# Kernel tuning notes

Measured on AMD Instinct MI355X. Metric: run time of the kernel, lower is better.

The kernel has to match this reference:

```python
import jax, jax.numpy as jnp
import numpy as np

NEG_INF = -1e9

def setup_inputs() -> dict:
    key = jax.random.key(0)
    ks = jax.random.split(key, 6)
    B, M, RNN, H, D = 64, 1024, 1024, 512, 2048
    return {
        "h": jax.random.normal(ks[0], (B, RNN), dtype=jnp.float32),
        "att_feats": jax.random.normal(ks[1], (B, M, D), dtype=jnp.float32),
        "att_mask": jax.random.randint(ks[2], (B, M), 0, 2, dtype=jnp.int32),
        "p_att_feats": jax.random.normal(ks[3], (B, M, H), dtype=jnp.float32),
        "W_ah": jax.random.normal(ks[4], (H, RNN), dtype=jnp.float32) * (1.0 / np.sqrt(RNN)),
        "w_alpha": jax.random.normal(ks[5], (H,), dtype=jnp.float32) * (1.0 / np.sqrt(H)),
    }

def reference(h, att_feats, att_mask, p_att_feats, W_ah, w_alpha):
    # Wah(h): [B, H]
    wah = h @ W_ah.T
    # additive attention energies: tanh(Wah(h)[:, None, :] + p_att_feats) -> [B, M, H]
    e = jnp.tanh(wah[:, None, :] + p_att_feats)
    # project to scalar per region: [B, M]
    logits = jnp.einsum("bmh,h->bm", e, w_alpha)
    logits = jnp.where(att_mask == 0, NEG_INF, logits)
    alpha = jax.nn.softmax(logits, axis=-1)
    # weighted sum of region features: [B, D]
    att = jnp.einsum("bm,bmd->bd", alpha, att_feats)
    return att
```

## Files before the change

kernel.cpp:

```cpp
#include <hip/hip_runtime.h>
#include <math.h>

#define B   64
#define M   1024
#define RNN 1024
#define H   512
#define D   2048
#define NEG_INF -1e9f

#define MBLK   8
#define MCHUNK (M / MBLK)

__device__ __forceinline__ float fast_tanh(float x) {
    float ax = fabsf(x);
    float t  = __expf(-2.0f * ax);
    float r  = (1.0f - t) / (1.0f + t);
    return copysignf(r, x);
}

__global__ __launch_bounds__(256) void k_wah(const float* __restrict__ h,
                                             const float* __restrict__ W,
                                             float* __restrict__ wah) {
    int wid  = (blockIdx.x * 256 + threadIdx.x) >> 6;
    int lane = threadIdx.x & 63;
    int b = wid >> 9;
    int j = wid & (H - 1);
    const float4* hp = (const float4*)(h + (size_t)b * RNN);
    const float4* wp = (const float4*)(W + (size_t)j * RNN);
    float acc = 0.0f;
#pragma unroll
    for (int t = 0; t < 4; ++t) {
        int i = lane + t * 64;
        float4 a = hp[i];
        float4 w = wp[i];
        acc += a.x * w.x + a.y * w.y + a.z * w.z + a.w * w.w;
    }
#pragma unroll
    for (int off = 32; off > 0; off >>= 1)
        acc += __shfl_down(acc, off);
    if (lane == 0) wah[wid] = acc;
}

__global__ __launch_bounds__(256) void k_logits(const float* __restrict__ wah,
                                                const float* __restrict__ p_att,
                                                const int* __restrict__ mask,
                                                const float* __restrict__ w_alpha,
                                                float* __restrict__ logits) {
    int row  = (blockIdx.x * 256 + threadIdx.x) >> 6;
    int lane = threadIdx.x & 63;
    int b = row >> 10;
    if (mask[row] == 0) {
        if (lane == 0) logits[row] = NEG_INF;
        return;
    }
    const float4* pp  = (const float4*)(p_att + (size_t)row * H);
    const float4* whp = (const float4*)(wah + (size_t)b * H);
    const float4* wap = (const float4*)w_alpha;
    float acc = 0.0f;
#pragma unroll
    for (int t = 0; t < 2; ++t) {
        int i = lane + t * 64;
        float4 p  = pp[i];
        float4 wh = whp[i];
        float4 wa = wap[i];
        acc += fast_tanh(p.x + wh.x) * wa.x;
        acc += fast_tanh(p.y + wh.y) * wa.y;
        acc += fast_tanh(p.z + wh.z) * wa.z;
        acc += fast_tanh(p.w + wh.w) * wa.w;
    }
#pragma unroll
    for (int off = 32; off > 0; off >>= 1)
        acc += __shfl_down(acc, off);
    if (lane == 0) logits[row] = acc;
}

__global__ __launch_bounds__(256) void k_att_partial(const float* __restrict__ logits,
                                                     const float* __restrict__ feats,
                                                     float* __restrict__ partial) {
    const int b    = blockIdx.x;
    const int dblk = blockIdx.y;
    const int mblk = blockIdx.z;
    const int tid  = threadIdx.x;
    const int lane = tid & 63;
    const int wid  = tid >> 6;

    __shared__ float s_logit[M];
    __shared__ float s_red[4];
    __shared__ float s_a[MCHUNK];
    __shared__ unsigned short s_idx[MCHUNK];
    __shared__ int s_c0, s_cnt;

    const float4* lg = (const float4*)(logits + (size_t)b * M);
    float4 v = lg[tid];
    ((float4*)s_logit)[tid] = v;
    float mx = fmaxf(fmaxf(v.x, v.y), fmaxf(v.z, v.w));
#pragma unroll
    for (int off = 32; off > 0; off >>= 1)
        mx = fmaxf(mx, __shfl_xor(mx, off));
    if (lane == 0) s_red[wid] = mx;
    __syncthreads();
    mx = fmaxf(fmaxf(s_red[0], s_red[1]), fmaxf(s_red[2], s_red[3]));

    float se = __expf(v.x - mx) + __expf(v.y - mx) + __expf(v.z - mx) + __expf(v.w - mx);
#pragma unroll
    for (int off = 32; off > 0; off >>= 1)
        se += __shfl_xor(se, off);
    __syncthreads();
    if (lane == 0) s_red[wid] = se;
    __syncthreads();
    const float inv = 1.0f / (s_red[0] + s_red[1] + s_red[2] + s_red[3]);

    float a = 0.0f;
    bool pred = false;
    if (tid < MCHUNK) {
        a = __expf(s_logit[mblk * MCHUNK + tid] - mx) * inv;
        pred = (a != 0.0f);
    }
    unsigned long long bal = __ballot(pred);
    int pos = __popcll(bal & ((1ull << lane) - 1ull));
    if (wid == 0 && lane == 0) s_c0 = __popcll(bal);
    if (wid == 0 && pred) { s_idx[pos] = (unsigned short)tid; s_a[pos] = a; }
    __syncthreads();
    const int c0 = s_c0;
    if (wid == 1 && pred) { s_idx[c0 + pos] = (unsigned short)(tid & 127); s_a[c0 + pos] = a; }
    if (wid == 1 && lane == 0) s_cnt = c0 + __popcll(bal);
    __syncthreads();
    const int cnt = s_cnt;

    const int d0 = dblk * 1024 + tid * 4;
    const float* fbase = feats + ((size_t)b * M + (size_t)mblk * MCHUNK) * D + d0;
    float4 acc = {0.f, 0.f, 0.f, 0.f};
    int i = 0;
    for (; i + 4 <= cnt; i += 4) {
        int m0 = s_idx[i], m1 = s_idx[i + 1], m2 = s_idx[i + 2], m3 = s_idx[i + 3];
        float a0 = s_a[i], a1 = s_a[i + 1], a2 = s_a[i + 2], a3 = s_a[i + 3];
        float4 f0 = *(const float4*)(fbase + (size_t)m0 * D);
        float4 f1 = *(const float4*)(fbase + (size_t)m1 * D);
        float4 f2 = *(const float4*)(fbase + (size_t)m2 * D);
        float4 f3 = *(const float4*)(fbase + (size_t)m3 * D);
        acc.x += a0 * f0.x; acc.y += a0 * f0.y; acc.z += a0 * f0.z; acc.w += a0 * f0.w;
        acc.x += a1 * f1.x; acc.y += a1 * f1.y; acc.z += a1 * f1.z; acc.w += a1 * f1.w;
        acc.x += a2 * f2.x; acc.y += a2 * f2.y; acc.z += a2 * f2.z; acc.w += a2 * f2.w;
        acc.x += a3 * f3.x; acc.y += a3 * f3.y; acc.z += a3 * f3.z; acc.w += a3 * f3.w;
    }
    for (; i < cnt; ++i) {
        int m0 = s_idx[i];
        float a0 = s_a[i];
        float4 f0 = *(const float4*)(fbase + (size_t)m0 * D);
        acc.x += a0 * f0.x; acc.y += a0 * f0.y; acc.z += a0 * f0.z; acc.w += a0 * f0.w;
    }
    *(float4*)(partial + ((size_t)mblk * B + b) * D + d0) = acc;
}

__global__ __launch_bounds__(256) void k_att_reduce(const float* __restrict__ partial,
                                                    float* __restrict__ out) {
    int i = blockIdx.x * 256 + threadIdx.x;
    float s = 0.0f;
#pragma unroll
    for (int mb = 0; mb < MBLK; ++mb)
        s += partial[(size_t)mb * (B * D) + i];
    out[i] = s;
}

extern "C" void kernel_launch(void* const* d_in, const int* in_sizes, int n_in,
                              void* d_out, int out_size, void* d_ws, size_t ws_size,
                              hipStream_t stream) {
    const float* h       = (const float*)d_in[0];
    const float* feats   = (const float*)d_in[1];
    const int*   mask    = (const int*)d_in[2];
    const float* p_att   = (const float*)d_in[3];
    const float* W_ah    = (const float*)d_in[4];
    const float* w_alpha = (const float*)d_in[5];
    float* out = (float*)d_out;

    float* ws      = (float*)d_ws;
    float* wah     = ws;
    float* logits  = wah + B * H;
    float* partial = logits + B * M;

    k_wah        <<<dim3(B * H / 4), 256, 0, stream>>>(h, W_ah, wah);
    k_logits     <<<dim3(B * M / 4), 256, 0, stream>>>(wah, p_att, mask, w_alpha, logits);
    k_att_partial<<<dim3(B, D / 1024, MBLK), 256, 0, stream>>>(logits, feats, partial);
    k_att_reduce <<<dim3(B * D / 256), 256, 0, stream>>>(partial, out);
}
```

Before: 82.18 us.

## Precompute compacted softmax entries once per batch and fuse weighted sum without partials

Softmax and compaction of nonzero attention weights now run once per batch row in a dedicated prep kernel that writes (byte offset, weight) pairs padded to a multiple of 16. Previously this was recomputed in every att_partial block. The gather kernel then reads all entries per batch in one pass with 16-way unrolled loads, which removes the partial buffer and the reduce kernel. It also swaps the tanh division for a hardware reciprocal. The trade-off is a lower grid size for the gather (256 blocks of 128 threads), which may reduce memory parallelism, plus an extra small kernel launch.

```diff
diff --git a/kernel.cpp b/kernel.cpp
--- a/kernel.cpp
+++ b/kernel.cpp
@@ -8,13 +8,10 @@
 #define D   2048
 #define NEG_INF -1e9f
 
-#define MBLK   8
-#define MCHUNK (M / MBLK)
-
 __device__ __forceinline__ float fast_tanh(float x) {
     float ax = fabsf(x);
     float t  = __expf(-2.0f * ax);
-    float r  = (1.0f - t) / (1.0f + t);
+    float r  = (1.0f - t) * __builtin_amdgcn_rcpf(1.0f + t);
     return copysignf(r, x);
 }
 
@@ -74,25 +71,18 @@
     if (lane == 0) logits[row] = acc;
 }
 
-__global__ __launch_bounds__(256) void k_att_partial(const float* __restrict__ logits,
-                                                     const float* __restrict__ feats,
-                                                     float* __restrict__ partial) {
-    const int b    = blockIdx.x;
-    const int dblk = blockIdx.y;
-    const int mblk = blockIdx.z;
-    const int tid  = threadIdx.x;
-    const int lane = tid & 63;
-    const int wid  = tid >> 6;
-
-    __shared__ float s_logit[M];
+__global__ __launch_bounds__(256) void k_prep(const float* __restrict__ logits,
+                                              uint2* __restrict__ ent,
+                                              int* __restrict__ cnt) {
+    const int b = blockIdx.x, tid = threadIdx.x;
+    const int lane = tid & 63, wid = tid >> 6;
+    __shared__ float s_al[M];
     __shared__ float s_red[4];
-    __shared__ float s_a[MCHUNK];
-    __shared__ unsigned short s_idx[MCHUNK];
-    __shared__ int s_c0, s_cnt;
+    __shared__ int   s_wcnt[16];
+    __shared__ int   s_base[17];
 
     const float4* lg = (const float4*)(logits + (size_t)b * M);
     float4 v = lg[tid];
-    ((float4*)s_logit)[tid] = v;
     float mx = fmaxf(fmaxf(v.x, v.y), fmaxf(v.z, v.w));
 #pragma unroll
     for (int off = 32; off > 0; off >>= 1)
@@ -101,7 +91,9 @@
     __syncthreads();
     mx = fmaxf(fmaxf(s_red[0], s_red[1]), fmaxf(s_red[2], s_red[3]));
 
-    float se = __expf(v.x - mx) + __expf(v.y - mx) + __expf(v.z - mx) + __expf(v.w - mx);
+    float e0 = __expf(v.x - mx), e1 = __expf(v.y - mx);
+    float e2 = __expf(v.z - mx), e3 = __expf(v.w - mx);
+    float se = e0 + e1 + e2 + e3;
 #pragma unroll
     for (int off = 32; off > 0; off >>= 1)
         se += __shfl_xor(se, off);
@@ -110,56 +102,81 @@
     __syncthreads();
     const float inv = 1.0f / (s_red[0] + s_red[1] + s_red[2] + s_red[3]);
 
-    float a = 0.0f;
-    bool pred = false;
-    if (tid < MCHUNK) {
-        a = __expf(s_logit[mblk * MCHUNK + tid] - mx) * inv;
-        pred = (a != 0.0f);
-    }
-    unsigned long long bal = __ballot(pred);
-    int pos = __popcll(bal & ((1ull << lane) - 1ull));
-    if (wid == 0 && lane == 0) s_c0 = __popcll(bal);
-    if (wid == 0 && pred) { s_idx[pos] = (unsigned short)tid; s_a[pos] = a; }
-    __syncthreads();
-    const int c0 = s_c0;
-    if (wid == 1 && pred) { s_idx[c0 + pos] = (unsigned short)(tid & 127); s_a[c0 + pos] = a; }
-    if (wid == 1 && lane == 0) s_cnt = c0 + __popcll(bal);
-    __syncthreads();
-    const int cnt = s_cnt;
-
-    const int d0 = dblk * 1024 + tid * 4;
-    const float* fbase = feats + ((size_t)b * M + (size_t)mblk * MCHUNK) * D + d0;
-    float4 acc = {0.f, 0.f, 0.f, 0.f};
-    int i = 0;
-    for (; i + 4 <= cnt; i += 4) {
-        int m0 = s_idx[i], m1 = s_idx[i + 1], m2 = s_idx[i + 2], m3 = s_idx[i + 3];
-        float a0 = s_a[i], a1 = s_a[i + 1], a2 = s_a[i + 2], a3 = s_a[i + 3];
-        float4 f0 = *(const float4*)(fbase + (size_t)m0 * D);
-        float4 f1 = *(const float4*)(fbase + (size_t)m1 * D);
-        float4 f2 = *(const float4*)(fbase + (size_t)m2 * D);
-        float4 f3 = *(const float4*)(fbase + (size_t)m3 * D);
-        acc.x += a0 * f0.x; acc.y += a0 * f0.y; acc.z += a0 * f0.z; acc.w += a0 * f0.w;
-        acc.x += a1 * f1.x; acc.y += a1 * f1.y; acc.z += a1 * f1.z; acc.w += a1 * f1.w;
-        acc.x += a2 * f2.x; acc.y += a2 * f2.y; acc.z += a2 * f2.z; acc.w += a2 * f2.w;
-        acc.x += a3 * f3.x; acc.y += a3 * f3.y; acc.z += a3 * f3.z; acc.w += a3 * f3.w;
-    }
-    for (; i < cnt; ++i) {
-        int m0 = s_idx[i];
-        float a0 = s_a[i];
-        float4 f0 = *(const float4*)(fbase + (size_t)m0 * D);
-        acc.x += a0 * f0.x; acc.y += a0 * f0.y; acc.z += a0 * f0.z; acc.w += a0 * f0.w;
-    }
-    *(float4*)(partial + ((size_t)mblk * B + b) * D + d0) = acc;
-}
-
-__global__ __launch_bounds__(256) void k_att_reduce(const float* __restrict__ partial,
-                                                    float* __restrict__ out) {
-    int i = blockIdx.x * 256 + threadIdx.x;
-    float s = 0.0f;
-#pragma unroll
-    for (int mb = 0; mb < MBLK; ++mb)
-        s += partial[(size_t)mb * (B * D) + i];
-    out[i] = s;
+    float4 av = {e0 * inv, e1 * inv, e2 * inv, e3 * inv};
+    ((float4*)s_al)[tid] = av;
+    __syncthreads();
+
+#pragma unroll
+    for (int p = 0; p < 4; ++p) {
+        float a = s_al[p * 256 + tid];
+        unsigned long long bal = __ballot(a != 0.0f);
+        if (lane == 0) s_wcnt[p * 4 + wid] = __popcll(bal);
+    }
+    __syncthreads();
+    if (tid == 0) {
+        int run = 0;
+#pragma unroll
+        for (int i = 0; i < 16; ++i) { s_base[i] = run; run += s_wcnt[i]; }
+        s_base[16] = run;
+        cnt[b] = (run + 15) & ~15;
+    }
+    __syncthreads();
+
+    uint2* eb = ent + (size_t)b * M;
+#pragma unroll
+    for (int p = 0; p < 4; ++p) {
+        int m = p * 256 + tid;
+        float a = s_al[m];
+        unsigned long long bal = __ballot(a != 0.0f);
+        int pos = __popcll(bal & ((1ull << lane) - 1ull));
+        if (a != 0.0f)
+            eb[s_base[p * 4 + wid] + pos] =
+                make_uint2((unsigned)(m * D * 4), __float_as_uint(a));
+    }
+    int total = s_base[16];
+    int padded = (total + 15) & ~15;
+    if (tid < 16 && total + tid < padded)
+        eb[total + tid] = make_uint2(0u, 0u);
+}
+
+__global__ __launch_bounds__(128) void k_att(const uint2* __restrict__ ent,
+                                             const int* __restrict__ cnt,
+                                             const float* __restrict__ feats,
+                                             float* __restrict__ out) {
+    const int b = blockIdx.x, dq = blockIdx.y;
+    const int tid = threadIdx.x;
+    const int d0 = dq * 512 + tid * 4;
+    const char* fbase = (const char*)(feats + (size_t)b * M * D + d0);
+    const uint2* eb = ent + (size_t)b * M;
+    const int n = cnt[b];
+
+    float4 acc[4];
+#pragma unroll
+    for (int c = 0; c < 4; ++c) acc[c] = make_float4(0.f, 0.f, 0.f, 0.f);
+
+    for (int i = 0; i < n; i += 16) {
+        uint2 e[16];
+#pragma unroll
+        for (int u = 0; u < 16; ++u) e[u] = eb[i + u];
+        float4 f[16];
+#pragma unroll
+        for (int u = 0; u < 16; ++u)
+            f[u] = *(const float4*)(fbase + e[u].x);
+#pragma unroll
+        for (int u = 0; u < 16; ++u) {
+            float a = __uint_as_float(e[u].y);
+            float4 F = f[u];
+            int c = u & 3;
+            acc[c].x += a * F.x; acc[c].y += a * F.y;
+            acc[c].z += a * F.z; acc[c].w += a * F.w;
+        }
+    }
+    float4 r;
+    r.x = (acc[0].x + acc[1].x) + (acc[2].x + acc[3].x);
+    r.y = (acc[0].y + acc[1].y) + (acc[2].y + acc[3].y);
+    r.z = (acc[0].z + acc[1].z) + (acc[2].z + acc[3].z);
+    r.w = (acc[0].w + acc[1].w) + (acc[2].w + acc[3].w);
+    *(float4*)(out + (size_t)b * D + d0) = r;
 }
 
 extern "C" void kernel_launch(void* const* d_in, const int* in_sizes, int n_in,
@@ -173,13 +190,14 @@
     const float* w_alpha = (const float*)d_in[5];
     float* out = (float*)d_out;
 
-    float* ws      = (float*)d_ws;
-    float* wah     = ws;
-    float* logits  = wah + B * H;
-    float* partial = logits + B * M;
-
-    k_wah        <<<dim3(B * H / 4), 256, 0, stream>>>(h, W_ah, wah);
-    k_logits     <<<dim3(B * M / 4), 256, 0, stream>>>(wah, p_att, mask, w_alpha, logits);
-    k_att_partial<<<dim3(B, D / 1024, MBLK), 256, 0, stream>>>(logits, feats, partial);
-    k_att_reduce <<<dim3(B * D / 256), 256, 0, stream>>>(partial, out);
-}
+    float* ws     = (float*)d_ws;
+    float* wah    = ws;
+    float* logits = wah + B * H;
+    uint2* ent    = (uint2*)(logits + B * M);
+    int*   cnt    = (int*)(ent + B * M);
+
+    k_wah   <<<dim3(B * H / 4), 256, 0, stream>>>(h, W_ah, wah);
+    k_logits<<<dim3(B * M / 4), 256, 0, stream>>>(wah, p_att, mask, w_alpha, logits);
+    k_prep  <<<dim3(B), 256, 0, stream>>>(logits, ent, cnt);
+    k_att   <<<dim3(B, 4), 128, 0, stream>>>(ent, cnt, feats, out);
+}
```

Result: slower. 89.94 us (+9.4%).
